# Optimization experiments

Hardware: AMD Instinct MI355X
Metric: run time of the kernel (lower is better)

## Reference

```python
import jax, jax.numpy as jnp
import numpy as np

C = 256   # channel
NH = 8    # n_heads
NP = 8    # n_points (n_levels = 1)
HD = C // NH


def conv1x1(x, W, b):
    # x: [B,C,H,W], W: [Cout,Cin] -> 1x1 conv == channel-mixing GEMM
    return jnp.einsum('bchw,oc->bohw', x, W) + b[None, :, None, None]


def linear(x, W, b):
    # x: [B,Q,Cin], W: [Cout,Cin] (torch nn.Linear layout)
    return jnp.einsum('bqc,oc->bqo', x, W) + b


def msda(value, loc, attn_w, H, Wd):
    # Multi-scale deformable attention core (single level).
    # value:  [B,Q,NH,HD]  (Q = H*Wd)
    # loc:    [B,Q,NH,NP,2] normalized sampling locations in [0,1] (x,y)
    # attn_w: [B,Q,NH,NP]  softmax weights
    B, Q = value.shape[0], value.shape[1]
    v = jnp.transpose(value, (0, 2, 1, 3))  # [B,NH,HW,HD]
    # grid_sample(align_corners=False): pixel coord = loc*size - 0.5
    ix = loc[..., 0] * Wd - 0.5
    iy = loc[..., 1] * H - 0.5
    x0 = jnp.floor(ix)
    y0 = jnp.floor(iy)

    def gather(xi, yi, wgt):
        valid = ((xi >= 0) & (xi < Wd) & (yi >= 0) & (yi < H)).astype(wgt.dtype)
        xc = jnp.clip(xi, 0, Wd - 1).astype(jnp.int32)
        yc = jnp.clip(yi, 0, H - 1).astype(jnp.int32)
        idx = yc * Wd + xc                                  # [B,Q,NH,NP]
        idx = jnp.transpose(idx, (0, 2, 1, 3)).reshape(B, NH, Q * NP)
        s = jnp.take_along_axis(v, idx[..., None], axis=2)  # [B,NH,Q*NP,HD]
        s = s.reshape(B, NH, Q, NP, HD)
        w = jnp.transpose(wgt * valid, (0, 2, 1, 3))[..., None]
        return s * w

    acc = (gather(x0, y0, (x0 + 1 - ix) * (y0 + 1 - iy))
           + gather(x0 + 1, y0, (ix - x0) * (y0 + 1 - iy))
           + gather(x0, y0 + 1, (x0 + 1 - ix) * (iy - y0))
           + gather(x0 + 1, y0 + 1, (ix - x0) * (iy - y0)))
    aw = jnp.transpose(attn_w, (0, 2, 1, 3))[..., None]      # [B,NH,Q,NP,1]
    out = (acc * aw).sum(axis=3)                             # [B,NH,Q,HD]
    return jnp.transpose(out, (0, 2, 1, 3)).reshape(B, Q, C)


def setup_inputs() -> dict:
    key = jax.random.key(0)
    ks = jax.random.split(key, 24)
    B, H, W = 2, 128, 128

    def w(k, shape, s=0.02):
        return jax.random.normal(k, shape, jnp.float32) * s

    d = {
        'xt': jax.random.normal(ks[0], (B, C, H, W), jnp.float32),
        'xt_1': jax.random.normal(ks[1], (B, C, H, W), jnp.float32),
        'W_in1': w(ks[2], (C, C)), 'b_in1': jnp.zeros((C,), jnp.float32),
        'W_in2': w(ks[3], (C, C)), 'b_in2': jnp.zeros((C,), jnp.float32),
        'Wv': w(ks[4], (C, C)), 'bv': jnp.zeros((C,), jnp.float32),
        'Ws': w(ks[5], (NH * NP * 2, C)), 'bs_off': w(ks[6], (NH * NP * 2,), 1.0),
        'Wa': w(ks[7], (NH * NP, C)), 'ba': jnp.zeros((NH * NP,), jnp.float32),
        'Wo': w(ks[8], (C, C)), 'bo': jnp.zeros((C,), jnp.float32),
        'Wt1': w(ks[9], (C, C)), 'bt1': jnp.zeros((C,), jnp.float32),
        'Wt2': w(ks[10], (C, C)), 'bt2': jnp.zeros((C,), jnp.float32),
        'Wout': w(ks[11], (C, C)), 'bout': jnp.zeros((C,), jnp.float32),
    }
    return d


def reference(xt, xt_1, W_in1, b_in1, W_in2, b_in2, Wv, bv, Ws, bs_off,
              Wa, ba, Wo, bo, Wt1, bt1, Wt2, bt2, Wout, bout):
    x1 = conv1x1(xt, W_in1, b_in1)
    x2 = conv1x1(xt_1, W_in2, b_in2)
    B, _, H, Wd = x1.shape
    Q = H * Wd
    q = jnp.transpose(x1, (0, 2, 3, 1)).reshape(B, Q, C)       # queries
    vflat = jnp.transpose(x2, (0, 2, 3, 1)).reshape(B, Q, C)   # values

    value = linear(vflat, Wv, bv).reshape(B, Q, NH, HD)
    offsets = linear(q, Ws, bs_off).reshape(B, Q, NH, NP, 2)
    attn = jax.nn.softmax(linear(q, Wa, ba).reshape(B, Q, NH, NP), axis=-1)

    # reference points at pixel centers, normalized (x,y)
    gy, gx = jnp.meshgrid(jnp.arange(H), jnp.arange(Wd), indexing='ij')
    ref = jnp.stack([(gx.reshape(-1) + 0.5) / Wd,
                     (gy.reshape(-1) + 0.5) / H], axis=-1).astype(jnp.float32)
    norm = jnp.array([Wd, H], jnp.float32)
    loc = ref[None, :, None, None, :] + offsets / norm          # [B,Q,NH,NP,2]

    out = msda(value, loc, attn, H, Wd)                         # [B,Q,C]
    xt_star = jnp.transpose(linear(out, Wo, bo), (0, 2, 1)).reshape(B, C, H, Wd)

    tg = conv1x1(jax.nn.relu(conv1x1(x1 * xt_star, Wt1, bt1)), Wt2, bt2)
    return jax.nn.relu(conv1x1(x1 + tg, Wout, bout))
```

## Files before the change

kernel.cpp:

```cpp
#include <hip/hip_runtime.h>
#include <math.h>


#define PIX 16384
#define BATCH 2
#define CH 256

typedef short bf16x8 __attribute__((ext_vector_type(8)));
typedef float f32x4 __attribute__((ext_vector_type(4)));

typedef const __attribute__((address_space(1))) void* as1cv;
typedef __attribute__((address_space(3))) void* as3v;
__device__ __forceinline__ void gl_lds16(const void* g, void* l) {
  __builtin_amdgcn_global_load_lds((as1cv)g, (as3v)l, 16, 0, 0);
}

__device__ __forceinline__ ushort f2bf(float f) {
  union { float f; unsigned u; } v; v.f = f;
  unsigned u = v.u;
  unsigned r = u + 0x7fffu + ((u >> 16) & 1u);
  return (ushort)(r >> 16);
}
__device__ __forceinline__ float bfl(unsigned u) {
  union { unsigned u; float f; } v; v.u = u << 16; return v.f;
}
__device__ __forceinline__ float bfh(unsigned u) {
  union { unsigned u; float f; } v; v.u = u & 0xffff0000u; return v.f;
}
__device__ __forceinline__ unsigned fuse_u32(unsigned a, unsigned b, bool mul) {
  float rl = mul ? bfl(a) * bfl(b) : bfl(a) + bfl(b);
  float rh = mul ? bfh(a) * bfh(b) : bfh(a) + bfh(b);
  return (unsigned)f2bf(rl) | ((unsigned)f2bf(rh) << 16);
}

__global__ __launch_bounds__(256) void prep_k(
    const float* __restrict__ xt, const float* __restrict__ xt_1,
    ushort* __restrict__ s0, ushort* __restrict__ s1,
    const float* __restrict__ W_in1, const float* __restrict__ Wo,
    const float* __restrict__ Wt1, const float* __restrict__ Wt2,
    const float* __restrict__ Wout, const float* __restrict__ Ws,
    const float* __restrict__ Wa, const float* __restrict__ bs_off,
    const float* __restrict__ ba, ushort* __restrict__ wb,
    float* __restrict__ bsa,
    const float* __restrict__ Wv, const float* __restrict__ W_in2,
    const float* __restrict__ b_in2, const float* __restrict__ bv,
    ushort* __restrict__ wvp, float* __restrict__ bvp)
{
  __shared__ float lds[32][33];
  const int bid = blockIdx.x;
  const int tid = threadIdx.x;

  if (bid < 16384) {
    const int z = bid >> 12;
    const int rem = bid & 4095;
    const int pblk = rem & 511, cblk = rem >> 9;
    const int b = z & 1;
    const float* in = (z < 2) ? xt : xt_1;
    ushort* out = (z < 2) ? s0 : s1;
    const int p0 = pblk * 32, c0 = cblk * 32;
    const int tx = tid & 31, ty = tid >> 5;
    const float* inb = in + (size_t)b * CH * PIX;
    #pragma unroll
    for (int i = 0; i < 4; ++i)
      lds[ty + i * 8][tx] = inb[(size_t)(c0 + ty + i * 8) * PIX + p0 + tx];
    __syncthreads();
    const int cx = (tid & 15) * 2, py = tid >> 4;
    ushort* outb = out + (size_t)b * PIX * CH;
    #pragma unroll
    for (int i = 0; i < 2; ++i) {
      int pl = py + i * 16;
      unsigned lo = f2bf(lds[cx][pl]);
      unsigned hi = f2bf(lds[cx + 1][pl]);
      *(unsigned*)(outb + (size_t)(p0 + pl) * CH + c0 + cx) = lo | (hi << 16);
    }
  } else if (bid < 16384 + 1473) {
    const int blk = bid - 16384;
    const int k = tid;
    if (blk >= 1472) {
      if (k < 128) bsa[k] = bs_off[k];
      else if (k < 192) bsa[k] = ba[k - 128];
      return;
    }
    const float* src;
    if (blk < 256) src = W_in1 + (size_t)blk * 256;
    else if (blk < 512) src = Wo + (size_t)(blk - 256) * 256;
    else if (blk < 768) src = Wt1 + (size_t)(blk - 512) * 256;
    else if (blk < 1024) src = Wt2 + (size_t)(blk - 768) * 256;
    else if (blk < 1280) src = Wout + (size_t)(blk - 1024) * 256;
    else if (blk < 1408) src = Ws + (size_t)(blk - 1280) * 256;
    else src = Wa + (size_t)(blk - 1408) * 256;
    wb[(size_t)blk * 256 + k] = f2bf(src[k]);
  } else {
    const int oo = bid - 17857;
    const int k = tid;
    float acc = 0.f;
    #pragma unroll 8
    for (int c = 0; c < 256; ++c)
      acc += Wv[(size_t)oo * 256 + c] * W_in2[(size_t)c * 256 + k];
    wvp[(size_t)oo * 256 + k] = f2bf(acc);
    float* red = &lds[0][0];
    red[k] = Wv[(size_t)oo * 256 + k] * b_in2[k];
    __syncthreads();
    for (int s = 128; s > 0; s >>= 1) {
      if (k < s) red[k] += red[k + s];
      __syncthreads();
    }
    if (k == 0) bvp[oo] = red[0] + bv[oo];
  }
}

template<bool RELU, int OMODE>
__global__ __launch_bounds__(256, 4) void gemm2p_k(
    const ushort* __restrict__ in, const ushort* __restrict__ Wb,
    const float* __restrict__ bias, void* __restrict__ out,
    int ldo, size_t obstride)
{
  __shared__ __align__(16) char smem[36864];
  const int tid = threadIdx.x;
  const int b = blockIdx.z;
  const int p0 = blockIdx.x * 128;
  const int o0 = blockIdx.y * 64;

  const ushort* inb = in + (size_t)b * PIX * CH;

  const int srow = tid >> 2;
  const int sseg = tid & 3;
  const int swz0 = (srow >> 1) & 3;
  const int swz1 = ((srow + 64) >> 1) & 3;
  const int gseg0 = sseg ^ swz0;
  const int gseg1 = sseg ^ swz1;
  const ushort* xsrc0 = inb + (size_t)(p0 + srow) * CH + gseg0 * 8;
  const ushort* xsrc1 = inb + (size_t)(p0 + srow + 64) * CH + gseg1 * 8;
  const ushort* wsrc = Wb + (size_t)(o0 + srow) * CH + gseg0 * 8;

  const int l = tid & 63, wv = tid >> 6;
  const int lr = l & 15, g4 = l >> 4;

  f32x4 acc[2][4];
  #pragma unroll
  for (int i = 0; i < 2; ++i)
    #pragma unroll
    for (int j = 0; j < 4; ++j) acc[i][j] = (f32x4){0.f, 0.f, 0.f, 0.f};

#define STAGE_P(buf, kb)                                                       \
  {                                                                            \
    gl_lds16(xsrc0 + (kb), smem + (buf) * 8192 + tid * 16);                    \
    gl_lds16(xsrc1 + (kb), smem + (buf) * 8192 + 4096 + tid * 16);             \
    gl_lds16(wsrc + (kb), smem + 24576 + (buf) * 4096 + tid * 16);             \
  }

  STAGE_P(0, 0)
  STAGE_P(1, 32)
  asm volatile("s_waitcnt vmcnt(3)" ::: "memory");
  __builtin_amdgcn_s_barrier();

  for (int t = 0; t < 8; ++t) {
    if (t < 6) STAGE_P((t + 2) % 3, (t + 2) * 32)
    const char* XB = smem + (t % 3) * 8192;
    const char* WB = smem + 24576 + (t % 3) * 4096;
    bf16x8 af[2], bfr[4];
    #pragma unroll
    for (int fm = 0; fm < 2; ++fm) {
      const int p = wv * 32 + fm * 16 + lr;
      af[fm] = *(const bf16x8*)(XB + p * 64 + ((g4 ^ ((p >> 1) & 3)) * 16));
    }
    #pragma unroll
    for (int fn = 0; fn < 4; ++fn) {
      const int o = fn * 16 + lr;
      bfr[fn] = *(const bf16x8*)(WB + o * 64 + ((g4 ^ ((o >> 1) & 3)) * 16));
    }
    #pragma unroll
    for (int fm = 0; fm < 2; ++fm)
      #pragma unroll
      for (int fn = 0; fn < 4; ++fn)
        acc[fm][fn] = __builtin_amdgcn_mfma_f32_16x16x32_bf16(af[fm], bfr[fn], acc[fm][fn], 0, 0, 0);
    if (t < 7) {
      if (t < 6) asm volatile("s_waitcnt vmcnt(3)" ::: "memory");
      else       asm volatile("s_waitcnt vmcnt(0)" ::: "memory");
      __builtin_amdgcn_s_barrier();
    }
  }
#undef STAGE_P
  __builtin_amdgcn_s_barrier();

  float bvv[4];
  #pragma unroll
  for (int fn = 0; fn < 4; ++fn) bvv[fn] = bias[o0 + fn * 16 + lr];

  ushort* El = (ushort*)smem;
  #pragma unroll
  for (int fm = 0; fm < 2; ++fm)
    #pragma unroll
    for (int fn = 0; fn < 4; ++fn)
      #pragma unroll
      for (int r = 0; r < 4; ++r) {
        const int p = wv * 32 + fm * 16 + g4 * 4 + r;
        float v = acc[fm][fn][r] + bvv[fn];
        if (RELU) v = fmaxf(v, 0.f);
        El[p * 72 + fn * 16 + lr] = f2bf(v);
      }
  __syncthreads();
  ushort* outb = (ushort*)out + (size_t)b * obstride;
  const int rg = tid >> 3, seg = tid & 7;
  #pragma unroll
  for (int r = 0; r < 4; ++r) {
    const int row = rg + r * 32;
    uint4 v = *(uint4*)(smem + row * 144 + seg * 16);
    *(uint4*)(outb + (size_t)(p0 + row) * ldo + o0 + seg * 8) = v;
  }
}

__global__ __launch_bounds__(256, 4) void gemm2p_dual_k(
    const ushort* __restrict__ inA, const ushort* __restrict__ inB,
    const ushort* __restrict__ WbA, const ushort* __restrict__ WbB,
    const float* __restrict__ biasA, const float* __restrict__ biasB,
    ushort* __restrict__ outA, ushort* __restrict__ outB)
{
  __shared__ __align__(16) char smem[36864];
  const int tid = threadIdx.x;
  const int b = blockIdx.z;
  const int p0 = blockIdx.x * 128;
  const bool second = blockIdx.y >= 4;
  const int o0 = (blockIdx.y & 3) * 64;
  const ushort* in = second ? inB : inA;
  const ushort* Wb = second ? WbB : WbA;
  const float* bias = second ? biasB : biasA;
  ushort* out = second ? outB : outA;

  const ushort* inb = in + (size_t)b * PIX * CH;

  const int srow = tid >> 2;
  const int sseg = tid & 3;
  const int swz0 = (srow >> 1) & 3;
  const int swz1 = ((srow + 64) >> 1) & 3;
  const int gseg0 = sseg ^ swz0;
  const int gseg1 = sseg ^ swz1;
  const ushort* xsrc0 = inb + (size_t)(p0 + srow) * CH + gseg0 * 8;
  const ushort* xsrc1 = inb + (size_t)(p0 + srow + 64) * CH + gseg1 * 8;
  const ushort* wsrc = Wb + (size_t)(o0 + srow) * CH + gseg0 * 8;

  const int l = tid & 63, wv = tid >> 6;
  const int lr = l & 15, g4 = l >> 4;

  f32x4 acc[2][4];
  #pragma unroll
  for (int i = 0; i < 2; ++i)
    #pragma unroll
    for (int j = 0; j < 4; ++j) acc[i][j] = (f32x4){0.f, 0.f, 0.f, 0.f};

#define STAGE_P(buf, kb)                                                       \
  {                                                                            \
    gl_lds16(xsrc0 + (kb), smem + (buf) * 8192 + tid * 16);                    \
    gl_lds16(xsrc1 + (kb), smem + (buf) * 8192 + 4096 + tid * 16);             \
    gl_lds16(wsrc + (kb), smem + 24576 + (buf) * 4096 + tid * 16);             \
  }

  STAGE_P(0, 0)
  STAGE_P(1, 32)
  asm volatile("s_waitcnt vmcnt(3)" ::: "memory");
  __builtin_amdgcn_s_barrier();

  for (int t = 0; t < 8; ++t) {
    if (t < 6) STAGE_P((t + 2) % 3, (t + 2) * 32)
    const char* XB = smem + (t % 3) * 8192;
    const char* WB = smem + 24576 + (t % 3) * 4096;
    bf16x8 af[2], bfr[4];
    #pragma unroll
    for (int fm = 0; fm < 2; ++fm) {
      const int p = wv * 32 + fm * 16 + lr;
      af[fm] = *(const bf16x8*)(XB + p * 64 + ((g4 ^ ((p >> 1) & 3)) * 16));
    }
    #pragma unroll
    for (int fn = 0; fn < 4; ++fn) {
      const int o = fn * 16 + lr;
      bfr[fn] = *(const bf16x8*)(WB + o * 64 + ((g4 ^ ((o >> 1) & 3)) * 16));
    }
    #pragma unroll
    for (int fm = 0; fm < 2; ++fm)
      #pragma unroll
      for (int fn = 0; fn < 4; ++fn)
        acc[fm][fn] = __builtin_amdgcn_mfma_f32_16x16x32_bf16(af[fm], bfr[fn], acc[fm][fn], 0, 0, 0);
    if (t < 7) {
      if (t < 6) asm volatile("s_waitcnt vmcnt(3)" ::: "memory");
      else       asm volatile("s_waitcnt vmcnt(0)" ::: "memory");
      __builtin_amdgcn_s_barrier();
    }
  }
#undef STAGE_P
  __builtin_amdgcn_s_barrier();

  float bvv[4];
  #pragma unroll
  for (int fn = 0; fn < 4; ++fn) bvv[fn] = bias[o0 + fn * 16 + lr];

  ushort* El = (ushort*)smem;
  #pragma unroll
  for (int fm = 0; fm < 2; ++fm)
    #pragma unroll
    for (int fn = 0; fn < 4; ++fn)
      #pragma unroll
      for (int r = 0; r < 4; ++r) {
        const int p = wv * 32 + fm * 16 + g4 * 4 + r;
        El[p * 72 + fn * 16 + lr] = f2bf(acc[fm][fn][r] + bvv[fn]);
      }
  __syncthreads();
  ushort* outb = out + (size_t)b * PIX * CH;
  const int rg = tid >> 3, seg = tid & 7;
  #pragma unroll
  for (int r = 0; r < 4; ++r) {
    const int row = rg + r * 32;
    uint4 v = *(uint4*)(smem + row * 144 + seg * 16);
    *(uint4*)(outb + (size_t)(p0 + row) * CH + o0 + seg * 8) = v;
  }
}

template<int FUSE, bool RELU, int OMODE>
__global__ __launch_bounds__(256, 4) void gemm2_k(
    const ushort* __restrict__ in, const ushort* __restrict__ in2,
    const ushort* __restrict__ Wb, const float* __restrict__ bias,
    void* __restrict__ out, int ldo, size_t obstride)
{
  constexpr int SMEMSZ = (OMODE == 0) ? 24576 : 34816;
  __shared__ __align__(16) char smem[SMEMSZ];
  const int tid = threadIdx.x;
  const int b = blockIdx.z;
  const int p0 = blockIdx.x * 128;
  const int o0 = blockIdx.y * 64;

  const ushort* inb = in + (size_t)b * PIX * CH;

  const int srow = tid >> 2;
  const int sseg = tid & 3;
  const int swz0 = (srow >> 1) & 3;
  const int swz1 = ((srow + 64) >> 1) & 3;
  const ushort* xsrc0 = inb + (size_t)(p0 + srow) * CH + sseg * 8;
  const ushort* xsrc1 = inb + (size_t)(p0 + srow + 64) * CH + sseg * 8;
  const ushort* x2src0 = in2 + (size_t)b * PIX * CH + (size_t)(p0 + srow) * CH + sseg * 8;
  const ushort* x2src1 = in2 + (size_t)b * PIX * CH + (size_t)(p0 + srow + 64) * CH + sseg * 8;
  const ushort* wsrc = Wb + (size_t)(o0 + srow) * CH + (sseg ^ swz0) * 8;

  const int l = tid & 63, wv = tid >> 6;
  const int lr = l & 15, g4 = l >> 4;

  f32x4 acc[2][4];
  #pragma unroll
  for (int i = 0; i < 2; ++i)
    #pragma unroll
    for (int j = 0; j < 4; ++j) acc[i][j] = (f32x4){0.f, 0.f, 0.f, 0.f};

  uint4 xr[2], x2r[2], wr;

#define LOADT(kb)                                                              \
  {                                                                            \
    xr[0] = *(const uint4*)(xsrc0 + (kb));                                     \
    xr[1] = *(const uint4*)(xsrc1 + (kb));                                     \
    x2r[0] = *(const uint4*)(x2src0 + (kb));                                   \
    x2r[1] = *(const uint4*)(x2src1 + (kb));                                   \
    wr = *(const uint4*)(wsrc + (kb));                                         \
  }

#define WRITET(buf)                                                            \
  {                                                                            \
    _Pragma("unroll")                                                          \
    for (int r = 0; r < 2; ++r) {                                              \
      uint4 v = xr[r];                                                         \
      unsigned* pa = (unsigned*)&v;                                            \
      const unsigned* pb = (const unsigned*)&x2r[r];                           \
      _Pragma("unroll")                                                        \
      for (int w = 0; w < 4; ++w) pa[w] = fuse_u32(pa[w], pb[w], FUSE == 1);   \
      const int sw = r ? swz1 : swz0;                                          \
      *(uint4*)(smem + (buf) * 8192 + r * 4096 + srow * 64 +                   \
                ((sseg ^ sw) * 16)) = v;                                       \
    }                                                                          \
    gl_lds16(wsrc + (buf##_kb), smem + 16384 + (buf) * 4096 + tid * 16);       \
  }

  int b0_kb, b1_kb; (void)b0_kb; (void)b1_kb;
  LOADT(0)
  b0_kb = 0;
  {
    _Pragma("unroll")
    for (int r = 0; r < 2; ++r) {
      uint4 v = xr[r];
      unsigned* pa = (unsigned*)&v;
      const unsigned* pb = (const unsigned*)&x2r[r];
      _Pragma("unroll")
      for (int w = 0; w < 4; ++w) pa[w] = fuse_u32(pa[w], pb[w], FUSE == 1);
      const int sw = r ? swz1 : swz0;
      *(uint4*)(smem + r * 4096 + srow * 64 + ((sseg ^ sw) * 16)) = v;
    }
    gl_lds16(wsrc + 0, smem + 16384 + tid * 16);
  }
  __syncthreads();

  for (int t = 0; t < 8; ++t) {
    if (t < 7) {
      LOADT((t + 1) * 32)
    }
    const char* XB = smem + (t & 1) * 8192;
    const char* WB = smem + 16384 + (t & 1) * 4096;
    bf16x8 af[2], bfr[4];
    #pragma unroll
    for (int fm = 0; fm < 2; ++fm) {
      const int p = wv * 32 + fm * 16 + lr;
      af[fm] = *(const bf16x8*)(XB + p * 64 + ((g4 ^ ((p >> 1) & 3)) * 16));
    }
    #pragma unroll
    for (int fn = 0; fn < 4; ++fn) {
      const int o = fn * 16 + lr;
      bfr[fn] = *(const bf16x8*)(WB + o * 64 + ((g4 ^ ((o >> 1) & 3)) * 16));
    }
    #pragma unroll
    for (int fm = 0; fm < 2; ++fm)
      #pragma unroll
      for (int fn = 0; fn < 4; ++fn)
        acc[fm][fn] = __builtin_amdgcn_mfma_f32_16x16x32_bf16(af[fm], bfr[fn], acc[fm][fn], 0, 0, 0);
    if (t < 7) {
      const int buf = (t + 1) & 1;
      _Pragma("unroll")
      for (int r = 0; r < 2; ++r) {
        uint4 v = xr[r];
        unsigned* pa = (unsigned*)&v;
        const unsigned* pb = (const unsigned*)&x2r[r];
        _Pragma("unroll")
        for (int w = 0; w < 4; ++w) pa[w] = fuse_u32(pa[w], pb[w], FUSE == 1);
        const int sw = r ? swz1 : swz0;
        *(uint4*)(smem + buf * 8192 + r * 4096 + srow * 64 + ((sseg ^ sw) * 16)) = v;
      }
      gl_lds16(wsrc + (t + 1) * 32, smem + 16384 + buf * 4096 + tid * 16);
    }
    __syncthreads();
  }
#undef LOADT
#undef WRITET

  float bvv[4];
  #pragma unroll
  for (int fn = 0; fn < 4; ++fn) bvv[fn] = bias[o0 + fn * 16 + lr];

  if (OMODE == 1) {
    float* El2 = (float*)smem;
    #pragma unroll
    for (int fm = 0; fm < 2; ++fm)
      #pragma unroll
      for (int fn = 0; fn < 4; ++fn) {
        float4 v;
        v.x = acc[fm][fn][0] + bvv[fn]; v.y = acc[fm][fn][1] + bvv[fn];
        v.z = acc[fm][fn][2] + bvv[fn]; v.w = acc[fm][fn][3] + bvv[fn];
        if (RELU) {
          v.x = fmaxf(v.x, 0.f); v.y = fmaxf(v.y, 0.f);
          v.z = fmaxf(v.z, 0.f); v.w = fmaxf(v.w, 0.f);
        }
        *(float4*)&El2[(size_t)(fn * 16 + lr) * 132 + wv * 32 + fm * 16 + g4 * 4] = v;
      }
    __syncthreads();
    float* outb = (float*)out + (size_t)b * obstride;
    const int og = tid >> 5, seg = tid & 31;
    #pragma unroll
    for (int r = 0; r < 8; ++r) {
      const int orow = og + r * 8;
      float4 v = *(float4*)(smem + orow * 528 + seg * 16);
      *(float4*)(outb + (size_t)(o0 + orow) * ldo + p0 + seg * 4) = v;
    }
  } else {
    ushort* El = (ushort*)smem;
    #pragma unroll
    for (int fm = 0; fm < 2; ++fm)
      #pragma unroll
      for (int fn = 0; fn < 4; ++fn)
        #pragma unroll
        for (int r = 0; r < 4; ++r) {
          const int p = wv * 32 + fm * 16 + g4 * 4 + r;
          float v = acc[fm][fn][r] + bvv[fn];
          if (RELU) v = fmaxf(v, 0.f);
          El[p * 72 + fn * 16 + lr] = f2bf(v);
        }
    __syncthreads();
    ushort* outb = (ushort*)out + (size_t)b * obstride;
    const int rg = tid >> 3, seg = tid & 7;
    #pragma unroll
    for (int r = 0; r < 4; ++r) {
      const int row = rg + r * 32;
      uint4 v = *(uint4*)(smem + row * 144 + seg * 16);
      *(uint4*)(outb + (size_t)(p0 + row) * ldo + o0 + seg * 8) = v;
    }
  }
}

__global__ __launch_bounds__(256) void msda_k(
    const ushort* __restrict__ value, const ushort* __restrict__ sa,
    ushort* __restrict__ out)
{
  const int t = blockIdx.x * 256 + threadIdx.x;
  const int dh = t & 1;
  const int h = (t >> 1) & 7;
  const int pg = t >> 4;
  const int b = pg >> 14;
  const int p = pg & (PIX - 1);
  const int px = p & 127, py = p >> 7;

  const ushort* vb = value + (size_t)b * PIX * CH;
  const ushort* sp = sa + (size_t)pg * 192;

  uint4 lgv = *(const uint4*)(sp + 128 + h * 8);
  const unsigned* lgw = (const unsigned*)&lgv;
  float lg[8];
  #pragma unroll
  for (int i = 0; i < 4; ++i) { lg[2 * i] = bfl(lgw[i]); lg[2 * i + 1] = bfh(lgw[i]); }
  float m = lg[0];
  #pragma unroll
  for (int i = 1; i < 8; ++i) m = fmaxf(m, lg[i]);
  float s = 0.f;
  #pragma unroll
  for (int i = 0; i < 8; ++i) { lg[i] = __expf(lg[i] - m); s += lg[i]; }
  const float inv = 1.f / s;

  uint4 ov0 = *(const uint4*)(sp + h * 16);
  uint4 ov1 = *(const uint4*)(sp + h * 16 + 8);
  float of[16];
  {
    const unsigned* ow = (const unsigned*)&ov0;
    #pragma unroll
    for (int i = 0; i < 4; ++i) { of[2 * i] = bfl(ow[i]); of[2 * i + 1] = bfh(ow[i]); }
    const unsigned* ow1 = (const unsigned*)&ov1;
    #pragma unroll
    for (int i = 0; i < 4; ++i) { of[8 + 2 * i] = bfl(ow1[i]); of[8 + 2 * i + 1] = bfh(ow1[i]); }
  }

  float acc[16];
  #pragma unroll
  for (int i = 0; i < 16; ++i) acc[i] = 0.f;

  #pragma unroll
  for (int pt = 0; pt < 8; ++pt) {
    const float ox = of[2 * pt], oy = of[2 * pt + 1];
    const float aw = lg[pt] * inv;
    const float ix = px + ox, iy = py + oy;
    const float xf = floorf(ix), yf = floorf(iy);
    const float fx = ix - xf, fy = iy - yf;
    const int x0 = (int)xf, y0 = (int)yf;
    #pragma unroll
    for (int cr = 0; cr < 4; ++cr) {
      const int dx = cr & 1, dy = cr >> 1;
      const int xx = x0 + dx, yy = y0 + dy;
      const float wx = dx ? fx : (1.f - fx);
      const float wy = dy ? fy : (1.f - fy);
      const bool valid = ((unsigned)xx < 128u) & ((unsigned)yy < 128u);
      float w = valid ? (wx * wy * aw) : 0.f;
      const int xc = min(max(xx, 0), 127), yc = min(max(yy, 0), 127);
      const ushort* vr = vb + ((size_t)(yc * 128 + xc) * CH + h * 32 + dh * 16);
      uint4 q0 = *(const uint4*)vr;
      uint4 q1 = *(const uint4*)(vr + 8);
      const unsigned* qw0 = (const unsigned*)&q0;
      const unsigned* qw1 = (const unsigned*)&q1;
      #pragma unroll
      for (int ww = 0; ww < 4; ++ww) {
        acc[2 * ww + 0] = fmaf(w, bfl(qw0[ww]), acc[2 * ww + 0]);
        acc[2 * ww + 1] = fmaf(w, bfh(qw0[ww]), acc[2 * ww + 1]);
        acc[8 + 2 * ww + 0] = fmaf(w, bfl(qw1[ww]), acc[8 + 2 * ww + 0]);
        acc[8 + 2 * ww + 1] = fmaf(w, bfh(qw1[ww]), acc[8 + 2 * ww + 1]);
      }
    }
  }
  unsigned r[8];
  #pragma unroll
  for (int k = 0; k < 8; ++k)
    r[k] = (unsigned)f2bf(acc[2 * k]) | ((unsigned)f2bf(acc[2 * k + 1]) << 16);
  ushort* dst = out + (size_t)pg * CH + h * 32 + dh * 16;
  *(uint4*)dst = *(uint4*)&r[0];
  *(uint4*)(dst + 8) = *(uint4*)&r[4];
}

extern "C" void kernel_launch(void* const* d_in, const int* in_sizes, int n_in,
                              void* d_out, int out_size, void* d_ws, size_t ws_size,
                              hipStream_t stream)
{
  const float* xt     = (const float*)d_in[0];
  const float* xt_1   = (const float*)d_in[1];
  const float* W_in1  = (const float*)d_in[2];
  const float* b_in1  = (const float*)d_in[3];
  const float* W_in2  = (const float*)d_in[4];
  const float* b_in2  = (const float*)d_in[5];
  const float* Wv     = (const float*)d_in[6];
  const float* bv     = (const float*)d_in[7];
  const float* Ws     = (const float*)d_in[8];
  const float* bs_off = (const float*)d_in[9];
  const float* Wa     = (const float*)d_in[10];
  const float* ba     = (const float*)d_in[11];
  const float* Wo     = (const float*)d_in[12];
  const float* bo     = (const float*)d_in[13];
  const float* Wt1    = (const float*)d_in[14];
  const float* bt1    = (const float*)d_in[15];
  const float* Wt2    = (const float*)d_in[16];
  const float* bt2    = (const float*)d_in[17];
  const float* Wout   = (const float*)d_in[18];
  const float* bout   = (const float*)d_in[19];

  char* ws = (char*)d_ws;
  const size_t SLOT = (size_t)BATCH * PIX * CH * 2;
  const size_t SAB  = (size_t)BATCH * PIX * 192 * 2;
  ushort* s0 = (ushort*)(ws + 0 * SLOT);
  ushort* s1 = (ushort*)(ws + 1 * SLOT);
  ushort* s2 = (ushort*)(ws + 2 * SLOT);
  ushort* s3 = (ushort*)(ws + 3 * SLOT);
  ushort* s4 = (ushort*)(ws + 4 * SLOT);
  ushort* sa = (ushort*)(ws + 5 * SLOT);
  char* wbase = ws + 5 * SLOT + SAB;
  ushort* wb  = (ushort*)wbase;
  ushort* wvp = (ushort*)(wbase + (size_t)1472 * 256 * 2);
  float* bsa  = (float*)(wbase + (size_t)1472 * 256 * 2 + (size_t)256 * 256 * 2);
  float* bvp  = bsa + 192;

  ushort* wb_in1 = wb;
  ushort* wb_o   = wb + 65536;
  ushort* wb_t1  = wb + 131072;
  ushort* wb_t2  = wb + 196608;
  ushort* wb_out = wb + 262144;
  ushort* wb_sa  = wb + 327680;

  dim3 blk(256);
  dim3 gD(PIX / 128, 8, BATCH);
  dim3 gF(PIX / 128, 4, BATCH);
  dim3 gS(PIX / 128, 3, BATCH);
  const size_t OBS = (size_t)PIX * CH;

  prep_k<<<18113, blk, 0, stream>>>(xt, xt_1, s0, s1,
      W_in1, Wo, Wt1, Wt2, Wout, Ws, Wa, bs_off, ba, wb, bsa,
      Wv, W_in2, b_in2, bv, wvp, bvp);

  gemm2p_dual_k<<<gD, blk, 0, stream>>>(s0, s1, wb_in1, wvp, b_in1, bvp, s2, s3);
  gemm2p_k<false, 0><<<gS, blk, 0, stream>>>(s2, wb_sa, bsa, sa, 192, (size_t)PIX * 192);
  msda_k<<<dim3((BATCH * PIX * 16) / 256), blk, 0, stream>>>(s3, sa, s4);
  gemm2p_k<false, 0><<<gF, blk, 0, stream>>>(s4, wb_o, bo, s0, CH, OBS);
  gemm2_k<1, true , 0><<<gF, blk, 0, stream>>>(s0, s2, wb_t1, bt1, s1, CH, OBS);
  gemm2p_k<false, 0><<<gF, blk, 0, stream>>>(s1, wb_t2, bt2, s3, CH, OBS);
  gemm2_k<2, true , 1><<<gF, blk, 0, stream>>>(s3, s2, wb_out, bout, d_out, PIX, (size_t)CH * PIX);
}
```

Baseline: 153.2 us.

## Deepen fused-input GEMM pipeline with triple-buffered weights and manual waitcnt barriers

Reworks the fused two-input GEMM main loop so activation tiles are prefetched two K-steps ahead into alternating register sets. Weight tiles go through a three-slot LDS ring via direct global-to-LDS loads. Full __syncthreads are replaced with explicit s_waitcnt vmcnt(5) plus s_barrier, so outstanding loads stay in flight across iterations and global latency is hidden better. The cost is more registers and LDS, with launch bounds lowered from 4 to 3 blocks per CU, and correctness now relies on hand-counted vmcnt values.

```diff
diff --git a/kernel.cpp b/kernel.cpp
--- a/kernel.cpp
+++ b/kernel.cpp
@@ -315,12 +315,12 @@
 }
 
 template<int FUSE, bool RELU, int OMODE>
-__global__ __launch_bounds__(256, 4) void gemm2_k(
+__global__ __launch_bounds__(256, 3) void gemm2f_k(
     const ushort* __restrict__ in, const ushort* __restrict__ in2,
     const ushort* __restrict__ Wb, const float* __restrict__ bias,
     void* __restrict__ out, int ldo, size_t obstride)
 {
-  constexpr int SMEMSZ = (OMODE == 0) ? 24576 : 34816;
+  constexpr int SMEMSZ = (OMODE == 0) ? 28672 : 34816;
   __shared__ __align__(16) char smem[SMEMSZ];
   const int tid = threadIdx.x;
   const int b = blockIdx.z;
@@ -328,6 +328,7 @@
   const int o0 = blockIdx.y * 64;
 
   const ushort* inb = in + (size_t)b * PIX * CH;
+  const ushort* in2b = in2 + (size_t)b * PIX * CH;
 
   const int srow = tid >> 2;
   const int sseg = tid & 3;
@@ -335,8 +336,8 @@
   const int swz1 = ((srow + 64) >> 1) & 3;
   const ushort* xsrc0 = inb + (size_t)(p0 + srow) * CH + sseg * 8;
   const ushort* xsrc1 = inb + (size_t)(p0 + srow + 64) * CH + sseg * 8;
-  const ushort* x2src0 = in2 + (size_t)b * PIX * CH + (size_t)(p0 + srow) * CH + sseg * 8;
-  const ushort* x2src1 = in2 + (size_t)b * PIX * CH + (size_t)(p0 + srow + 64) * CH + sseg * 8;
+  const ushort* x2src0 = in2b + (size_t)(p0 + srow) * CH + sseg * 8;
+  const ushort* x2src1 = in2b + (size_t)(p0 + srow + 64) * CH + sseg * 8;
   const ushort* wsrc = Wb + (size_t)(o0 + srow) * CH + (sseg ^ swz0) * 8;
 
   const int l = tid & 63, wv = tid >> 6;
@@ -348,18 +349,20 @@
     #pragma unroll
     for (int j = 0; j < 4; ++j) acc[i][j] = (f32x4){0.f, 0.f, 0.f, 0.f};
 
-  uint4 xr[2], x2r[2], wr;
-
-#define LOADT(kb)                                                              \
+  uint4 xrE[2], x2rE[2], xrO[2], x2rO[2];
+
+#define LOADX(kb, xr, x2r)                                                     \
   {                                                                            \
     xr[0] = *(const uint4*)(xsrc0 + (kb));                                     \
     xr[1] = *(const uint4*)(xsrc1 + (kb));                                     \
     x2r[0] = *(const uint4*)(x2src0 + (kb));                                   \
     x2r[1] = *(const uint4*)(x2src1 + (kb));                                   \
-    wr = *(const uint4*)(wsrc + (kb));                                         \
-  }
-
-#define WRITET(buf)                                                            \
+  }
+
+#define GLW(buf, kb)                                                           \
+  gl_lds16(wsrc + (kb), smem + 16384 + (buf) * 4096 + tid * 16);
+
+#define WRITEX(buf, xr, x2r)                                                   \
   {                                                                            \
     _Pragma("unroll")                                                          \
     for (int r = 0; r < 2; ++r) {                                              \
@@ -372,33 +375,26 @@
       *(uint4*)(smem + (buf) * 8192 + r * 4096 + srow * 64 +                   \
                 ((sseg ^ sw) * 16)) = v;                                       \
     }                                                                          \
-    gl_lds16(wsrc + (buf##_kb), smem + 16384 + (buf) * 4096 + tid * 16);       \
-  }
-
-  int b0_kb, b1_kb; (void)b0_kb; (void)b1_kb;
-  LOADT(0)
-  b0_kb = 0;
-  {
-    _Pragma("unroll")
-    for (int r = 0; r < 2; ++r) {
-      uint4 v = xr[r];
-      unsigned* pa = (unsigned*)&v;
-      const unsigned* pb = (const unsigned*)&x2r[r];
-      _Pragma("unroll")
-      for (int w = 0; w < 4; ++w) pa[w] = fuse_u32(pa[w], pb[w], FUSE == 1);
-      const int sw = r ? swz1 : swz0;
-      *(uint4*)(smem + r * 4096 + srow * 64 + ((sseg ^ sw) * 16)) = v;
-    }
-    gl_lds16(wsrc + 0, smem + 16384 + tid * 16);
-  }
-  __syncthreads();
-
+  }
+
+  LOADX(0, xrE, x2rE)
+  GLW(0, 0)
+  LOADX(32, xrO, x2rO)
+  GLW(1, 32)
+  WRITEX(0, xrE, x2rE)
+  asm volatile("s_waitcnt vmcnt(5) lgkmcnt(0)" ::: "memory");
+  __builtin_amdgcn_s_barrier();
+  __builtin_amdgcn_sched_barrier(0);
+
+  #pragma unroll
   for (int t = 0; t < 8; ++t) {
-    if (t < 7) {
-      LOADT((t + 1) * 32)
+    if (t < 6) {
+      if ((t & 1) == 0) { LOADX((t + 2) * 32, xrE, x2rE) }
+      else              { LOADX((t + 2) * 32, xrO, x2rO) }
+      GLW((t + 2) % 3, (t + 2) * 32)
     }
     const char* XB = smem + (t & 1) * 8192;
-    const char* WB = smem + 16384 + (t & 1) * 4096;
+    const char* WB = smem + 16384 + (t % 3) * 4096;
     bf16x8 af[2], bfr[4];
     #pragma unroll
     for (int fm = 0; fm < 2; ++fm) {
@@ -416,23 +412,18 @@
       for (int fn = 0; fn < 4; ++fn)
         acc[fm][fn] = __builtin_amdgcn_mfma_f32_16x16x32_bf16(af[fm], bfr[fn], acc[fm][fn], 0, 0, 0);
     if (t < 7) {
-      const int buf = (t + 1) & 1;
-      _Pragma("unroll")
-      for (int r = 0; r < 2; ++r) {
-        uint4 v = xr[r];
-        unsigned* pa = (unsigned*)&v;
-        const unsigned* pb = (const unsigned*)&x2r[r];
-        _Pragma("unroll")
-        for (int w = 0; w < 4; ++w) pa[w] = fuse_u32(pa[w], pb[w], FUSE == 1);
-        const int sw = r ? swz1 : swz0;
-        *(uint4*)(smem + buf * 8192 + r * 4096 + srow * 64 + ((sseg ^ sw) * 16)) = v;
-      }
-      gl_lds16(wsrc + (t + 1) * 32, smem + 16384 + buf * 4096 + tid * 16);
-    }
-    __syncthreads();
-  }
-#undef LOADT
-#undef WRITET
+      if (((t + 1) & 1) == 0) { WRITEX((t + 1) & 1, xrE, x2rE) }
+      else                    { WRITEX((t + 1) & 1, xrO, x2rO) }
+      if (t < 6) asm volatile("s_waitcnt vmcnt(5) lgkmcnt(0)" ::: "memory");
+      else       asm volatile("s_waitcnt vmcnt(0) lgkmcnt(0)" ::: "memory");
+      __builtin_amdgcn_s_barrier();
+      __builtin_amdgcn_sched_barrier(0);
+    }
+  }
+#undef LOADX
+#undef GLW
+#undef WRITEX
+  __syncthreads();
 
   float bvv[4];
   #pragma unroll
@@ -632,7 +623,7 @@
   gemm2p_k<false, 0><<<gS, blk, 0, stream>>>(s2, wb_sa, bsa, sa, 192, (size_t)PIX * 192);
   msda_k<<<dim3((BATCH * PIX * 16) / 256), blk, 0, stream>>>(s3, sa, s4);
   gemm2p_k<false, 0><<<gF, blk, 0, stream>>>(s4, wb_o, bo, s0, CH, OBS);
-  gemm2_k<1, true , 0><<<gF, blk, 0, stream>>>(s0, s2, wb_t1, bt1, s1, CH, OBS);
+  gemm2f_k<1, true , 0><<<gF, blk, 0, stream>>>(s0, s2, wb_t1, bt1, s1, CH, OBS);
   gemm2p_k<false, 0><<<gF, blk, 0, stream>>>(s1, wb_t2, bt2, s3, CH, OBS);
-  gemm2_k<2, true , 1><<<gF, blk, 0, stream>>>(s3, s2, wb_out, bout, d_out, PIX, (size_t)CH * PIX);
-}
+  gemm2f_k<2, true , 1><<<gF, blk, 0, stream>>>(s3, s2, wb_out, bout, d_out, PIX, (size_t)CH * PIX);
+}
```

Measured after the change: 153.6 us. About the same (+0.3%).
